# Optimization experiments

Hardware: AMD Instinct MI355X
Metric: run time of the kernel (lower is better)

Reference implementation:

```python
import jax, jax.numpy as jnp
import numpy as np

K = 21                     # kernel_size
LAM = 128.0                # lam
SIGMA_SPACE = 32.0
SIGMA_LUMA = 8.0
H = 512
W = 512
HO = H - K + 1             # valid conv output height (492)
WO = W - K + 1
C = (K - 1) // 2           # center offset (10)
CTR = C * K + C            # center channel index in row-major K*K patches


def _diff_patches(x):
    """x: (H, W) float. Returns (K*K-1, HO, WO): center pixel minus each
    of the other K*K-1 window taps (== the sparse 2-tap conv in torch)."""
    p = jax.lax.conv_general_dilated_patches(
        x[None, None], (K, K), (1, 1), 'VALID')[0]      # (K*K, HO, WO)
    diffs = p[CTR][None] - p                             # center - neighbor
    return jnp.delete(diffs, CTR, axis=0)                # drop all-zero center chan


def _make_w_ij(ref_hwc):
    """Bilateral affinity weights, per the torch __init__."""
    pos_x = jnp.broadcast_to(jnp.arange(W, dtype=jnp.float32)[None, :], (H, W))
    pos_y = jnp.broadcast_to(jnp.arange(H, dtype=jnp.float32)[:, None], (H, W))
    dx = _diff_patches(pos_x)
    dy = _diff_patches(pos_y)
    log_w = -(dx * dx + dy * dy) / (2.0 * SIGMA_SPACE ** 2)
    for c in range(ref_hwc.shape[-1]):                   # fixed 3 channels
        dr = _diff_patches(ref_hwc[:, :, c])
        log_w = log_w - dr * dr / (2.0 * SIGMA_LUMA ** 2)
    return jnp.exp(log_w)                                # (K*K-1, HO, WO)


def setup_inputs() -> dict:
    key = jax.random.key(0)
    k1, k2, k3 = jax.random.split(key, 3)
    output = jax.random.uniform(k1, (H, W), dtype=jnp.float32)   # logits/255
    target = jax.random.uniform(k2, (H, W), dtype=jnp.float32)   # target/255
    ref = jax.random.uniform(k3, (H, W, 3), dtype=jnp.float32) * 255.0
    w_ij = _make_w_ij(ref)
    bias = jnp.zeros((K * K - 1,), dtype=jnp.float32)   # torch conv bias (zeroed)
    return {"output": output, "target": target, "w_ij": w_ij, "bias": bias}


def reference(output, target, w_ij, bias):
    d = _diff_patches(output) + bias[:, None, None]      # (K*K-1, HO, WO)
    smooth = (H * W) * LAM * jnp.mean(w_ij * d * d)
    fidelity = jnp.mean((output - target) ** 2)
    return smooth + fidelity
```

## Files before the change

### kernel.cpp

```cpp
#include <hip/hip_runtime.h>

constexpr int Kk   = 21;
constexpr int Hh   = 512, Ww = 512;
constexpr int HO   = 492, WO = 492;
constexpr int Cc   = 10;
constexpr int CTRi = 220;
constexpr int NCH  = 440;
constexpr int ROW4 = WO / 4;
constexpr int N4F  = Hh * Ww / 4;

constexpr int SLABS     = 6;
constexpr int SLAB_ROWS = HO / SLABS;
constexpr int ITERS     = SLAB_ROWS / 2;
constexpr int NBLK      = NCH * SLABS;

constexpr float SCALE_S  = (float)((512.0 * 512.0 * 128.0) / (440.0 * 492.0 * 492.0));
constexpr float FID_RATIO = (float)((1.0 / (512.0 * 512.0)) /
                                    ((512.0 * 512.0 * 128.0) / (440.0 * 492.0 * 492.0)));

typedef float floatx4  __attribute__((ext_vector_type(4)));
typedef float floatx4u __attribute__((ext_vector_type(4), aligned(4)));

#define TPB 256

__device__ __forceinline__ float block_reduce_256(float v) {
    #pragma unroll
    for (int off = 32; off; off >>= 1) v += __shfl_down(v, off, 64);
    __shared__ float smem[TPB / 64];
    const int lane = threadIdx.x & 63;
    const int wid  = threadIdx.x >> 6;
    if (lane == 0) smem[wid] = v;
    __syncthreads();
    float r = 0.f;
    if (threadIdx.x == 0) {
        #pragma unroll
        for (int k = 0; k < TPB / 64; ++k) r += smem[k];
    }
    return r;
}

__global__ __launch_bounds__(TPB) void main_kernel(
        const float* __restrict__ outp,
        const float* __restrict__ targ,
        const float* __restrict__ w,
        const float* __restrict__ bias,
        float* __restrict__ partial)
{
    const int t = threadIdx.x;
    float acc = 0.f;

    {
        const int fq = blockIdx.x * TPB + t;
        if (fq < N4F) {
            const floatx4 a  = ((const floatx4*)outp)[fq];
            const floatx4 tg = ((const floatx4*)targ)[fq];
            const float d0 = a.x - tg.x, d1 = a.y - tg.y,
                        d2 = a.z - tg.z, d3 = a.w - tg.w;
            acc = (d0 * d0 + d1 * d1 + d2 * d2 + d3 * d3) * FID_RATIO;
        }
    }

    const int plane = blockIdx.x / SLABS;
    const int slab  = blockIdx.x % SLABS;

    if (t < 2 * ROW4) {
        const int kk = plane + (plane >= CTRi ? 1 : 0);
        const int ki = kk / Kk;
        const int kj = kk - ki * Kk;
        const float b = bias[plane];

        const int i0 = slab * SLAB_ROWS;
        const int r  = t / ROW4;
        const int j  = 4 * (t - r * ROW4);

        const floatx4* wp = (const floatx4*)w + ((long)plane * HO + i0) * ROW4 + t;
        const float* cp = outp + (i0 + r + Cc) * Ww + (Cc + j);
        const float* np = outp + (i0 + r + ki) * Ww + (kj + j);

        float a0 = 0.f, a1 = 0.f, a2 = 0.f, a3 = 0.f;
        #pragma unroll 4
        for (int it = 0; it < ITERS; ++it) {
            const floatx4  w4 = __builtin_nontemporal_load(wp);
            const floatx4u c4 = *(const floatx4u*)cp;
            const floatx4u n4 = *(const floatx4u*)np;

            const float d0 = c4.x - n4.x + b;
            const float d1 = c4.y - n4.y + b;
            const float d2 = c4.z - n4.z + b;
            const float d3 = c4.w - n4.w + b;

            a0 += w4.x * d0 * d0;
            a1 += w4.y * d1 * d1;
            a2 += w4.z * d2 * d2;
            a3 += w4.w * d3 * d3;

            wp += 2 * ROW4;
            cp += 2 * Ww;
            np += 2 * Ww;
        }
        acc += (a0 + a1) + (a2 + a3);
    }

    const float bsum = block_reduce_256(acc);
    if (t == 0) partial[blockIdx.x] = bsum;
}

__global__ __launch_bounds__(TPB) void finalize_kernel(
        const float* __restrict__ partial,
        float* __restrict__ out)
{
    float v = 0.f;
    for (int idx = threadIdx.x; idx < NBLK; idx += TPB) v += partial[idx];
    const float s = block_reduce_256(v);
    if (threadIdx.x == 0) out[0] = s * SCALE_S;
}

extern "C" void kernel_launch(void* const* d_in, const int* in_sizes, int n_in,
                              void* d_out, int out_size, void* d_ws, size_t ws_size,
                              hipStream_t stream) {
    const float* outp = (const float*)d_in[0];
    const float* targ = (const float*)d_in[1];
    const float* w    = (const float*)d_in[2];
    const float* bias = (const float*)d_in[3];

    float* partial = (float*)d_ws;

    main_kernel<<<NBLK, TPB, 0, stream>>>(outp, targ, w, bias, partial);
    finalize_kernel<<<1, TPB, 0, stream>>>(partial, (float*)d_out);
}
```

Before: 562.9 us.

## Distribute row-pair jobs across a fixed grid with grid-stride loop

Replaces the plane-by-slab block mapping (2640 blocks, each looping over a slab of rows in one plane) with a fixed grid of 1024 blocks that stride over all plane/row-pair jobs. Idle threads are clamped to a valid index and their weight is masked to zero instead of being branched around. The aim is more even load balance and fewer blocks launched, at the cost of per-iteration index division, the bias load, and a wider scatter of accesses across planes.

```diff
diff --git a/kernel.cpp b/kernel.cpp
--- a/kernel.cpp
+++ b/kernel.cpp
@@ -9,10 +9,9 @@
 constexpr int ROW4 = WO / 4;
 constexpr int N4F  = Hh * Ww / 4;
 
-constexpr int SLABS     = 6;
-constexpr int SLAB_ROWS = HO / SLABS;
-constexpr int ITERS     = SLAB_ROWS / 2;
-constexpr int NBLK      = NCH * SLABS;
+constexpr int JPP  = HO / 2;
+constexpr int JOBS = NCH * JPP;
+constexpr int NBLK = 1024;
 
 constexpr float SCALE_S  = (float)((512.0 * 512.0 * 128.0) / (440.0 * 492.0 * 492.0));
 constexpr float FID_RATIO = (float)((1.0 / (512.0 * 512.0)) /
@@ -60,46 +59,44 @@
         }
     }
 
-    const int plane = blockIdx.x / SLABS;
-    const int slab  = blockIdx.x % SLABS;
+    const int  te  = (t < 2 * ROW4) ? t : (2 * ROW4 - 1);
+    const float mk = (t < 2 * ROW4) ? 1.f : 0.f;
+    const int  r   = (te >= ROW4) ? 1 : 0;
+    const int  j   = 4 * (te - r * ROW4);
+    const int  co  = (r + Cc) * Ww + Cc + j;
 
-    if (t < 2 * ROW4) {
-        const int kk = plane + (plane >= CTRi ? 1 : 0);
-        const int ki = kk / Kk;
-        const int kj = kk - ki * Kk;
-        const float b = bias[plane];
+    float a0 = 0.f, a1 = 0.f, a2 = 0.f, a3 = 0.f;
 
-        const int i0 = slab * SLAB_ROWS;
-        const int r  = t / ROW4;
-        const int j  = 4 * (t - r * ROW4);
+    #pragma unroll 2
+    for (int v = blockIdx.x; v < JOBS; v += NBLK) {
+        const int plane = v / JPP;
+        const int rp    = v - plane * JPP;
+        const int kk    = plane + (plane >= CTRi ? 1 : 0);
+        const int ki    = kk / Kk;
+        const int kj    = kk - ki * Kk;
+        const float b   = bias[plane];
 
-        const floatx4* wp = (const floatx4*)w + ((long)plane * HO + i0) * ROW4 + t;
-        const float* cp = outp + (i0 + r + Cc) * Ww + (Cc + j);
-        const float* np = outp + (i0 + r + ki) * Ww + (kj + j);
+        const floatx4 w4 = __builtin_nontemporal_load(
+                (const floatx4*)w + (long)v * (2 * ROW4) + te);
 
-        float a0 = 0.f, a1 = 0.f, a2 = 0.f, a3 = 0.f;
-        #pragma unroll 4
-        for (int it = 0; it < ITERS; ++it) {
-            const floatx4  w4 = __builtin_nontemporal_load(wp);
-            const floatx4u c4 = *(const floatx4u*)cp;
-            const floatx4u n4 = *(const floatx4u*)np;
+        const float* base = outp + 2 * rp * Ww;
+        const floatx4u c4 = *(const floatx4u*)(base + co);
+        const floatx4u n4 = *(const floatx4u*)(base + (r + ki) * Ww + kj + j);
 
-            const float d0 = c4.x - n4.x + b;
-            const float d1 = c4.y - n4.y + b;
-            const float d2 = c4.z - n4.z + b;
-            const float d3 = c4.w - n4.w + b;
+        const float wm0 = w4.x * mk, wm1 = w4.y * mk,
+                    wm2 = w4.z * mk, wm3 = w4.w * mk;
 
-            a0 += w4.x * d0 * d0;
-            a1 += w4.y * d1 * d1;
-            a2 += w4.z * d2 * d2;
-            a3 += w4.w * d3 * d3;
+        const float d0 = c4.x - n4.x + b;
+        const float d1 = c4.y - n4.y + b;
+        const float d2 = c4.z - n4.z + b;
+        const float d3 = c4.w - n4.w + b;
 
-            wp += 2 * ROW4;
-            cp += 2 * Ww;
-            np += 2 * Ww;
-        }
-        acc += (a0 + a1) + (a2 + a3);
+        a0 += wm0 * d0 * d0;
+        a1 += wm1 * d1 * d1;
+        a2 += wm2 * d2 * d2;
+        a3 += wm3 * d3 * d3;
     }
+    acc += (a0 + a1) + (a2 + a3);
 
     const float bsum = block_reduce_256(acc);
     if (t == 0) partial[blockIdx.x] = bsum;
```

Result: no change. 560.9 us (-0.4%).
